# Performance work log

Measured on AMD Instinct MI355X. Metric: run time of the kernel, lower is better.

## Reference

```python
import jax, jax.numpy as jnp
import numpy as np

K = 16
NUM_CLASSES = 1000
TAU = 0.2
LOGIT_SCALE = 20.0


def setup_inputs() -> dict:
    key = jax.random.key(0)
    k1, k2, k3, k4, k5 = jax.random.split(key, 5)
    B, D, N = 2048, 256, 100000
    x = jax.random.normal(k1, (B, D), dtype=jnp.float32)
    mean = jax.random.normal(k2, (D,), dtype=jnp.float32)
    std = jax.random.uniform(k3, (D,), dtype=jnp.float32, minval=0.5, maxval=1.5)
    mem_features = jax.random.normal(k4, (N, D), dtype=jnp.float32)
    mem_labels = jax.random.randint(k5, (N,), 0, NUM_CLASSES)
    return {"x": x, "mean": mean, "std": std,
            "mem_features": mem_features, "mem_labels": mem_labels}


def reference(x, mean, std, mem_features, mem_labels):
    # preprocess: standardize then L2-normalize rows (eval mode, no noise)
    x = (x - mean) / std
    norm = jnp.maximum(jnp.linalg.norm(x, axis=1, keepdims=True), 1e-6)
    x = x / norm
    # dense cosine similarity: [B, N]
    sims = jnp.einsum('bd,nd->bn', x, mem_features)
    # top-k neighbors per query
    top_sims, top_idx = jax.lax.top_k(sims, K)          # [B, K]
    top_lbl = mem_labels[top_idx]                       # [B, K]
    weights = jax.nn.softmax(top_sims / max(1e-6, TAU), axis=1)
    # scatter-add softmax weights into class logits
    B = x.shape[0]
    rows = jnp.arange(B)[:, None]                       # [B, 1]
    logits = jnp.zeros((B, NUM_CLASSES), dtype=x.dtype).at[rows, top_lbl].add(weights)
    return logits * LOGIT_SCALE
```

## Files before the change

kernel.cpp:

```cpp
#include <hip/hip_runtime.h>
#include <math.h>

constexpr int BQ   = 2048;
constexpr int D    = 256;
constexpr int NMEM = 100000;
constexpr int TOPK = 16;
constexpr int NCLS = 1000;
constexpr float TAU = 0.2f;
constexpr float LOGIT_SCALE = 20.0f;

constexpr int KTOT = 256;
constexpr int BK   = 64;
constexpr int TM   = 128;
constexpr int TN   = 128;
constexpr int CTILES = 17;
constexpr int CHUNK  = TN * CTILES;
constexpr int NCH    = 48;
constexpr int RBLK   = BQ / TM;
constexpr int NBLK   = RBLK * NCH;
constexpr int TOTAL_IT = CTILES * (KTOT / BK);
constexpr float XSCALE = 16.0f;
constexpr float INV_XS = 0.0625f;
constexpr float THR    = 3.0f;
constexpr float THRS   = 48.0f;
constexpr int CAP    = 512;
constexpr int MSEL   = 64;
constexpr int SELCAP = 96;
constexpr float NEG  = -3.0e38f;

using i32x4  = __attribute__((ext_vector_type(4))) int;
using i32x8  = __attribute__((ext_vector_type(8))) int;
using f32x16 = __attribute__((ext_vector_type(16))) float;

__device__ __forceinline__ unsigned f2e4m3(float f) {
    const unsigned u = __float_as_uint(f);
    const unsigned s = (u >> 24) & 0x80u;
    const int e = (int)((u >> 23) & 0xff);
    int te = e - 120;
    if (te <= 0) return s;
    const unsigned m = u & 0x7fffffu;
    const unsigned r = m + 0x7ffffu + ((m >> 20) & 1u);
    unsigned keep;
    if (r & 0x800000u) { ++te; keep = 0; } else keep = (r >> 20) & 7u;
    if (te >= 16 || (te == 15 && keep == 7)) return s | 0x7eu;
    return s | ((unsigned)te << 3) | keep;
}

__device__ __forceinline__ void load_lds16(const void* g, void* l) {
    __builtin_amdgcn_global_load_lds((const __attribute__((address_space(1))) void*)g,
                                     (__attribute__((address_space(3))) void*)l,
                                     16, 0, 0);
}

__global__ __launch_bounds__(256) void knn_prep(
    const float* __restrict__ x, const float* __restrict__ mean,
    const float* __restrict__ stdv, unsigned char* __restrict__ A1,
    float* __restrict__ XN, int* __restrict__ cnt)
{
    const int row = blockIdx.x;
    const int t = threadIdx.x;
    float v = (x[row * D + t] - mean[t]) / stdv[t];
    float s = v * v;
    #pragma unroll
    for (int off = 32; off > 0; off >>= 1) s += __shfl_down(s, off, 64);
    __shared__ float wsum[4];
    __shared__ float nrm;
    const int lane = t & 63, wid = t >> 6;
    if (lane == 0) wsum[wid] = s;
    __syncthreads();
    if (t == 0) {
        nrm = fmaxf(sqrtf(wsum[0] + wsum[1] + wsum[2] + wsum[3]), 1e-6f);
        cnt[row] = 0;
    }
    __syncthreads();
    const float xnv = v / nrm;
    A1[(size_t)row * KTOT + t] = (unsigned char)f2e4m3(xnv * XSCALE);
    XN[(size_t)row * D + t] = xnv;
}

__global__ __launch_bounds__(256) void knn_convb(
    const float* __restrict__ mem, unsigned char* __restrict__ B1)
{
    const int tid = threadIdx.x;
    const int rloc = tid >> 5, t = tid & 31;
    const long n = (long)blockIdx.x * 8 + rloc;
    if (n >= NMEM) return;
    const float* src = mem + n * D + t * 8;
    const float4 v0 = *(const float4*)(src);
    const float4 v1 = *(const float4*)(src + 4);
    const float f[8] = {v0.x, v0.y, v0.z, v0.w, v1.x, v1.y, v1.z, v1.w};
    unsigned long long pk = 0;
    #pragma unroll
    for (int i = 0; i < 8; ++i)
        pk |= (unsigned long long)f2e4m3(f[i]) << (8 * i);
    *(unsigned long long*)(B1 + n * KTOT + t * 8) = pk;
}

__global__ __launch_bounds__(256, 3) void knn_gemm_topk(
    const unsigned char* __restrict__ A1, const unsigned char* __restrict__ B1,
    int* __restrict__ cnt, uint2* __restrict__ cand_buf)
{
    __shared__ alignas(16) unsigned char Bs[3][TN * BK];

    const int tid  = threadIdx.x;
    const int lane = tid & 63, wave = tid >> 6;
    const int wm = wave >> 1, wn = wave & 1;
    const int l31 = lane & 31;
    const int kb  = lane >> 5;

    const int nblk = blockIdx.x;
    const int xcd = nblk & 7, bi = nblk >> 3;
    const int rb = bi & 15;
    const int ch = (bi >> 4) + 6 * xcd;
    const int row0  = rb * TM;
    const int cbase = ch * CHUNK;

    i32x8 Areg[2][4];
    #pragma unroll
    for (int ti = 0; ti < 2; ++ti) {
        const unsigned char* ar =
            A1 + (size_t)(row0 + wm * 64 + ti * 32 + l31) * KTOT + kb * 32;
        #pragma unroll
        for (int ks = 0; ks < 4; ++ks) {
            const i32x4 lo = *(const i32x4*)(ar + ks * 64);
            const i32x4 hi = *(const i32x4*)(ar + ks * 64 + 16);
            Areg[ti][ks] = __builtin_shufflevector(lo, hi, 0, 1, 2, 3, 4, 5, 6, 7);
        }
    }

    int boff[2][2];
    #pragma unroll
    for (int tj = 0; tj < 2; ++tj) {
        const int br = wn * 64 + tj * 32 + l31;
        #pragma unroll
        for (int c = 0; c < 2; ++c)
            boff[tj][c] = br * BK + (((2 * kb + c) - (br >> 1)) & 3) * 16;
    }

    int cSub[2], bSeg[2];
    #pragma unroll
    for (int s = 0; s < 2; ++s) {
        const int ci = s * 256 + tid;
        const int r = ci >> 2, sl = ci & 3;
        cSub[s] = r;
        bSeg[s] = ((sl + (r >> 1)) & 3) << 4;
    }
    const unsigned char* bB[2];
    auto computeBB = [&](int tile) {
        #pragma unroll
        for (int s = 0; s < 2; ++s) {
            int candi = cbase + tile * TN + cSub[s];
            if (candi >= NMEM) candi = NMEM - 1;
            bB[s] = B1 + (size_t)candi * KTOT + bSeg[s];
        }
    };
    auto stageB = [&](int buf, int kofs) {
        #pragma unroll
        for (int s = 0; s < 2; ++s)
            load_lds16(bB[s] + kofs, (char*)Bs[buf] + s * 4096 + wave * 1024);
    };

    f32x16 acc[2][2];
    #pragma unroll
    for (int i = 0; i < 2; ++i)
        #pragma unroll
        for (int j = 0; j < 2; ++j)
            #pragma unroll
            for (int r = 0; r < 16; ++r) acc[i][j][r] = 0.f;

    computeBB(0);
    stageB(0, 0);
    stageB(1, 64);
    asm volatile("s_waitcnt vmcnt(2)" ::: "memory");
    __builtin_amdgcn_sched_barrier(0);
    __builtin_amdgcn_s_barrier();

    int p = 0;
    for (int t = 0; t < CTILES; ++t) {
        #pragma unroll
        for (int ks = 0; ks < 4; ++ks) {
            const int g = t * 4 + ks;

            const unsigned char* Bb = Bs[p];
            i32x8 Bfr[2];
            #pragma unroll
            for (int tj = 0; tj < 2; ++tj) {
                const i32x4 blo = *(const i32x4*)(Bb + boff[tj][0]);
                const i32x4 bhi = *(const i32x4*)(Bb + boff[tj][1]);
                Bfr[tj] = __builtin_shufflevector(blo, bhi, 0, 1, 2, 3, 4, 5, 6, 7);
            }

            const bool have2 = (g + 2 < TOTAL_IT);
            if (have2) {
                if (ks == 2) computeBB(t + 1);
                int pn = p + 2; if (pn >= 3) pn -= 3;
                stageB(pn, ((ks + 2) & 3) << 6);
            }

            #pragma unroll
            for (int ti = 0; ti < 2; ++ti)
                #pragma unroll
                for (int tj = 0; tj < 2; ++tj)
                    acc[ti][tj] = __builtin_amdgcn_mfma_scale_f32_32x32x64_f8f6f4(
                        Areg[ti][ks], Bfr[tj], acc[ti][tj], 0, 0,
                        0, 0x7f7f7f7f, 0, 0x7f7f7f7f);

            if (ks == 3) {
                const int tb = cbase + t * TN;
                #pragma unroll
                for (int ti = 0; ti < 2; ++ti) {
                    const int rb0 = row0 + wm * 64 + ti * 32 + 4 * kb;
                    #pragma unroll
                    for (int tj = 0; tj < 2; ++tj) {
                        const int cidx = tb + wn * 64 + tj * 32 + l31;
                        #pragma unroll
                        for (int r = 0; r < 16; ++r) {
                            const float v = acc[ti][tj][r];
                            if (v > THRS && cidx < NMEM) {
                                const int rg = rb0 + (r & 3) + 8 * (r >> 2);
                                const int pos = atomicAdd(&cnt[rg], 1);
                                if (pos < CAP)
                                    cand_buf[(size_t)rg * CAP + pos] =
                                        make_uint2(__float_as_uint(v * INV_XS),
                                                   (unsigned)cidx);
                            }
                            acc[ti][tj][r] = 0.f;
                        }
                    }
                }
            }

            if (g < TOTAL_IT - 1) {
                if (have2) {
                    asm volatile("s_waitcnt vmcnt(2)" ::: "memory");
                } else {
                    asm volatile("s_waitcnt vmcnt(0)" ::: "memory");
                }
                __builtin_amdgcn_sched_barrier(0);
                __builtin_amdgcn_s_barrier();
            }
            ++p; if (p >= 3) p = 0;
        }
    }
}

__global__ __launch_bounds__(256) void knn_final(
    const int* __restrict__ cnt, const uint2* __restrict__ cand_buf,
    const float* __restrict__ xn, const float* __restrict__ mem,
    const int* __restrict__ labels, float* __restrict__ out)
{
    constexpr float BSCALE = 200.0f;
    __shared__ float cls[NCLS];
    __shared__ uint2 cl[CAP];
    __shared__ int   hist[1024];
    __shared__ int   psum[256];
    __shared__ float tstar;
    __shared__ int   scount;
    __shared__ int   seli[SELCAP];
    __shared__ float ex[SELCAP];
    __shared__ float fs[TOPK];
    __shared__ int   fi[TOPK];
    __shared__ float zshare;

    const int row = blockIdx.x;
    const int tid = threadIdx.x;
    const int lane = tid & 63, w = tid >> 6;

    const float4 xr = *(const float4*)(xn + (size_t)row * D + lane * 4);

    for (int c = tid; c < NCLS; c += 256) cls[c] = 0.f;
    for (int i = tid; i < 1024; i += 256) hist[i] = 0;
    int n = cnt[row]; if (n > CAP) n = CAP;
    for (int i = tid; i < n; i += 256) cl[i] = cand_buf[(size_t)row * CAP + i];
    if (tid == 0) scount = 0;
    __syncthreads();

    for (int i = tid; i < n; i += 256) {
        const float v = __uint_as_float(cl[i].x);
        int b = (int)((v - THR) * BSCALE);
        b = max(0, min(1023, b));
        atomicAdd(&hist[b], 1);
    }
    __syncthreads();
    psum[tid] = hist[4 * tid] + hist[4 * tid + 1] + hist[4 * tid + 2] + hist[4 * tid + 3];
    __syncthreads();
    if (tid == 0) {
        int cum = 0, g = 255;
        for (; g >= 0; --g) {
            if (cum + psum[g] >= MSEL) break;
            cum += psum[g];
        }
        float t = THR;
        if (g >= 0) {
            int bb = 4 * g + 3;
            for (; bb > 4 * g; --bb) {
                cum += hist[bb];
                if (cum >= MSEL) break;
            }
            if (bb == 4 * g) cum += hist[bb];
            t = THR + (float)bb * (1.0f / BSCALE);
        }
        tstar = t;
    }
    __syncthreads();
    for (int i = tid; i < n; i += 256) {
        const float v = __uint_as_float(cl[i].x);
        if (v >= tstar) {
            const int p = atomicAdd(&scount, 1);
            if (p < SELCAP) seli[p] = (int)cl[i].y;
        }
    }
    __syncthreads();
    int ns = scount; if (ns > SELCAP) ns = SELCAP;

    for (int c = w; c < ns; c += 4) {
        const float4 mv = *(const float4*)(mem + (size_t)seli[c] * D + lane * 4);
        float s = xr.x * mv.x + xr.y * mv.y + xr.z * mv.z + xr.w * mv.w;
        #pragma unroll
        for (int off = 32; off > 0; off >>= 1) s += __shfl_down(s, off, 64);
        if (lane == 0) ex[c] = s;
    }
    __syncthreads();

    if (tid == 0) {
        float kmin = NEG; int kslot = 0;
        #pragma unroll
        for (int s = 0; s < TOPK; ++s) { fs[s] = NEG; fi[s] = -1; }
        for (int c = 0; c < ns; ++c) {
            const float v = ex[c];
            if (v > kmin) {
                fs[kslot] = v; fi[kslot] = seli[c];
                kmin = fs[0]; kslot = 0;
                #pragma unroll
                for (int s = 1; s < TOPK; ++s) {
                    const float tq = fs[s];
                    if (tq < kmin) { kmin = tq; kslot = s; }
                }
            }
        }
        float smax = fs[0];
        #pragma unroll
        for (int s = 1; s < TOPK; ++s) smax = fmaxf(smax, fs[s]);
        float e[TOPK]; float Z = 0.f;
        #pragma unroll
        for (int s = 0; s < TOPK; ++s) {
            e[s] = (fi[s] >= 0) ? expf((fs[s] - smax) * (1.0f / TAU)) : 0.f;
            Z += e[s];
        }
        for (int s = 0; s < TOPK; ++s) {
            if (fi[s] >= 0) cls[labels[fi[s]]] += e[s];
        }
        zshare = Z;
    }
    __syncthreads();
    const float scale = LOGIT_SCALE / zshare;
    for (int c = tid; c < NCLS; c += 256)
        out[(size_t)row * NCLS + c] = cls[c] * scale;
}

extern "C" void kernel_launch(void* const* d_in, const int* in_sizes, int n_in,
                              void* d_out, int out_size, void* d_ws, size_t ws_size,
                              hipStream_t stream) {
    (void)in_sizes; (void)n_in; (void)out_size; (void)ws_size;
    const float* x    = (const float*)d_in[0];
    const float* mean = (const float*)d_in[1];
    const float* stdv = (const float*)d_in[2];
    const float* mem  = (const float*)d_in[3];
    const int*   lbl  = (const int*)d_in[4];
    float* out = (float*)d_out;

    unsigned char* A1 = (unsigned char*)d_ws;
    float* XN = (float*)(A1 + (size_t)BQ * KTOT);
    unsigned char* B1 = (unsigned char*)(XN + (size_t)BQ * D);
    int* cnt = (int*)(B1 + (size_t)NMEM * KTOT);
    uint2* cand = (uint2*)(cnt + BQ);

    knn_prep<<<BQ, 256, 0, stream>>>(x, mean, stdv, A1, XN, cnt);
    knn_convb<<<(NMEM + 7) / 8, 256, 0, stream>>>(mem, B1);
    knn_gemm_topk<<<NBLK, 256, 0, stream>>>(A1, B1, cnt, cand);
    knn_final<<<BQ, 256, 0, stream>>>(cnt, cand, XN, mem, lbl, out);
}
```

Baseline: 420.7 us.

## Load B fragments directly from global into registers, drop LDS staging

The GEMM+threshold kernel stops staging memory-bank tiles through a triple-buffered LDS ring with barriers. Each wave now loads its B fragments straight from global into registers with a simple two-register double buffer. Blocks grow to 512 threads (8 waves, each owning 32 rows), and the chunk layout changes to 32 chunks of 25 tiles. This removes LDS traffic and block-wide barriers, at the cost of redundant global/L2 reads of B across waves and more exposed load latency without an explicit pipeline.

Result: slower. 466.9 us (+11.0%).

```diff
diff --git a/kernel.cpp b/kernel.cpp
--- a/kernel.cpp
+++ b/kernel.cpp
@@ -10,15 +10,13 @@
 constexpr float LOGIT_SCALE = 20.0f;
 
 constexpr int KTOT = 256;
-constexpr int BK   = 64;
 constexpr int TM   = 128;
 constexpr int TN   = 128;
-constexpr int CTILES = 17;
+constexpr int CTILES = 25;
 constexpr int CHUNK  = TN * CTILES;
-constexpr int NCH    = 48;
+constexpr int NCH    = 32;
 constexpr int RBLK   = BQ / TM;
 constexpr int NBLK   = RBLK * NCH;
-constexpr int TOTAL_IT = CTILES * (KTOT / BK);
 constexpr float XSCALE = 16.0f;
 constexpr float INV_XS = 0.0625f;
 constexpr float THR    = 3.0f;
@@ -44,12 +42,6 @@
     if (r & 0x800000u) { ++te; keep = 0; } else keep = (r >> 20) & 7u;
     if (te >= 16 || (te == 15 && keep == 7)) return s | 0x7eu;
     return s | ((unsigned)te << 3) | keep;
-}
-
-__device__ __forceinline__ void load_lds16(const void* g, void* l) {
-    __builtin_amdgcn_global_load_lds((const __attribute__((address_space(1))) void*)g,
-                                     (__attribute__((address_space(3))) void*)l,
-                                     16, 0, 0);
 }
 
 __global__ __launch_bounds__(256) void knn_prep(
@@ -96,12 +88,10 @@
     *(unsigned long long*)(B1 + n * KTOT + t * 8) = pk;
 }
 
-__global__ __launch_bounds__(256, 3) void knn_gemm_topk(
+__global__ __launch_bounds__(512, 4) void knn_gemm_topk(
     const unsigned char* __restrict__ A1, const unsigned char* __restrict__ B1,
     int* __restrict__ cnt, uint2* __restrict__ cand_buf)
 {
-    __shared__ alignas(16) unsigned char Bs[3][TN * BK];
-
     const int tid  = threadIdx.x;
     const int lane = tid & 63, wave = tid >> 6;
     const int wm = wave >> 1, wn = wave & 1;
@@ -111,135 +101,92 @@
     const int nblk = blockIdx.x;
     const int xcd = nblk & 7, bi = nblk >> 3;
     const int rb = bi & 15;
-    const int ch = (bi >> 4) + 6 * xcd;
+    const int ch = (bi >> 4) + 4 * xcd;
     const int row0  = rb * TM;
     const int cbase = ch * CHUNK;
 
-    i32x8 Areg[2][4];
-    #pragma unroll
-    for (int ti = 0; ti < 2; ++ti) {
+    i32x8 Areg[4];
+    {
         const unsigned char* ar =
-            A1 + (size_t)(row0 + wm * 64 + ti * 32 + l31) * KTOT + kb * 32;
+            A1 + (size_t)(row0 + wm * 32 + l31) * KTOT + kb * 32;
         #pragma unroll
         for (int ks = 0; ks < 4; ++ks) {
             const i32x4 lo = *(const i32x4*)(ar + ks * 64);
             const i32x4 hi = *(const i32x4*)(ar + ks * 64 + 16);
-            Areg[ti][ks] = __builtin_shufflevector(lo, hi, 0, 1, 2, 3, 4, 5, 6, 7);
-        }
-    }
-
-    int boff[2][2];
+            Areg[ks] = __builtin_shufflevector(lo, hi, 0, 1, 2, 3, 4, 5, 6, 7);
+        }
+    }
+
+    const int laneoff = wn * 64 + l31;
+    const unsigned char* bA[2];
+    auto computeBT = [&](int tile) {
+        const int tb = cbase + tile * TN;
+        #pragma unroll
+        for (int tj = 0; tj < 2; ++tj) {
+            int c = tb + laneoff + tj * 32;
+            if (c > NMEM - 1) c = NMEM - 1;
+            bA[tj] = B1 + ((size_t)c << 8) + kb * 32;
+        }
+    };
+    auto loadB = [&](int ksOfs, i32x8* dst) {
+        #pragma unroll
+        for (int tj = 0; tj < 2; ++tj) {
+            const i32x4 lo = *(const i32x4*)(bA[tj] + ksOfs);
+            const i32x4 hi = *(const i32x4*)(bA[tj] + ksOfs + 16);
+            dst[tj] = __builtin_shufflevector(lo, hi, 0, 1, 2, 3, 4, 5, 6, 7);
+        }
+    };
+
+    f32x16 acc[2];
     #pragma unroll
-    for (int tj = 0; tj < 2; ++tj) {
-        const int br = wn * 64 + tj * 32 + l31;
-        #pragma unroll
-        for (int c = 0; c < 2; ++c)
-            boff[tj][c] = br * BK + (((2 * kb + c) - (br >> 1)) & 3) * 16;
-    }
-
-    int cSub[2], bSeg[2];
-    #pragma unroll
-    for (int s = 0; s < 2; ++s) {
-        const int ci = s * 256 + tid;
-        const int r = ci >> 2, sl = ci & 3;
-        cSub[s] = r;
-        bSeg[s] = ((sl + (r >> 1)) & 3) << 4;
-    }
-    const unsigned char* bB[2];
-    auto computeBB = [&](int tile) {
-        #pragma unroll
-        for (int s = 0; s < 2; ++s) {
-            int candi = cbase + tile * TN + cSub[s];
-            if (candi >= NMEM) candi = NMEM - 1;
-            bB[s] = B1 + (size_t)candi * KTOT + bSeg[s];
-        }
-    };
-    auto stageB = [&](int buf, int kofs) {
-        #pragma unroll
-        for (int s = 0; s < 2; ++s)
-            load_lds16(bB[s] + kofs, (char*)Bs[buf] + s * 4096 + wave * 1024);
-    };
-
-    f32x16 acc[2][2];
-    #pragma unroll
-    for (int i = 0; i < 2; ++i)
-        #pragma unroll
-        for (int j = 0; j < 2; ++j)
+    for (int tj = 0; tj < 2; ++tj)
+        #pragma unroll
+        for (int r = 0; r < 16; ++r) acc[tj][r] = 0.f;
+
+    i32x8 Bb[2], Bc[2];
+    computeBT(0);
+    loadB(0, Bb);
+
+    for (int t = 0; t < CTILES; ++t) {
+        loadB(64, Bc);
+        #pragma unroll
+        for (int tj = 0; tj < 2; ++tj)
+            acc[tj] = __builtin_amdgcn_mfma_scale_f32_32x32x64_f8f6f4(
+                Areg[0], Bb[tj], acc[tj], 0, 0, 0, 0x7f7f7f7f, 0, 0x7f7f7f7f);
+        loadB(128, Bb);
+        #pragma unroll
+        for (int tj = 0; tj < 2; ++tj)
+            acc[tj] = __builtin_amdgcn_mfma_scale_f32_32x32x64_f8f6f4(
+                Areg[1], Bc[tj], acc[tj], 0, 0, 0, 0x7f7f7f7f, 0, 0x7f7f7f7f);
+        loadB(192, Bc);
+        #pragma unroll
+        for (int tj = 0; tj < 2; ++tj)
+            acc[tj] = __builtin_amdgcn_mfma_scale_f32_32x32x64_f8f6f4(
+                Areg[2], Bb[tj], acc[tj], 0, 0, 0, 0x7f7f7f7f, 0, 0x7f7f7f7f);
+        if (t + 1 < CTILES) { computeBT(t + 1); loadB(0, Bb); }
+        #pragma unroll
+        for (int tj = 0; tj < 2; ++tj)
+            acc[tj] = __builtin_amdgcn_mfma_scale_f32_32x32x64_f8f6f4(
+                Areg[3], Bc[tj], acc[tj], 0, 0, 0, 0x7f7f7f7f, 0, 0x7f7f7f7f);
+
+        const int tb = cbase + t * TN;
+        const int rb0 = row0 + wm * 32 + 4 * kb;
+        #pragma unroll
+        for (int tj = 0; tj < 2; ++tj) {
+            const int cidx = tb + wn * 64 + tj * 32 + l31;
             #pragma unroll
-            for (int r = 0; r < 16; ++r) acc[i][j][r] = 0.f;
-
-    computeBB(0);
-    stageB(0, 0);
-    stageB(1, 64);
-    asm volatile("s_waitcnt vmcnt(2)" ::: "memory");
-    __builtin_amdgcn_sched_barrier(0);
-    __builtin_amdgcn_s_barrier();
-
-    int p = 0;
-    for (int t = 0; t < CTILES; ++t) {
-        #pragma unroll
-        for (int ks = 0; ks < 4; ++ks) {
-            const int g = t * 4 + ks;
-
-            const unsigned char* Bb = Bs[p];
-            i32x8 Bfr[2];
-            #pragma unroll
-            for (int tj = 0; tj < 2; ++tj) {
-                const i32x4 blo = *(const i32x4*)(Bb + boff[tj][0]);
-                const i32x4 bhi = *(const i32x4*)(Bb + boff[tj][1]);
-                Bfr[tj] = __builtin_shufflevector(blo, bhi, 0, 1, 2, 3, 4, 5, 6, 7);
+            for (int r = 0; r < 16; ++r) {
+                const float v = acc[tj][r];
+                if (v > THRS && cidx < NMEM) {
+                    const int rg = rb0 + (r & 3) + 8 * (r >> 2);
+                    const int pos = atomicAdd(&cnt[rg], 1);
+                    if (pos < CAP)
+                        cand_buf[(size_t)rg * CAP + pos] =
+                            make_uint2(__float_as_uint(v * INV_XS),
+                                       (unsigned)cidx);
+                }
+                acc[tj][r] = 0.f;
             }
-
-            const bool have2 = (g + 2 < TOTAL_IT);
-            if (have2) {
-                if (ks == 2) computeBB(t + 1);
-                int pn = p + 2; if (pn >= 3) pn -= 3;
-                stageB(pn, ((ks + 2) & 3) << 6);
-            }
-
-            #pragma unroll
-            for (int ti = 0; ti < 2; ++ti)
-                #pragma unroll
-                for (int tj = 0; tj < 2; ++tj)
-                    acc[ti][tj] = __builtin_amdgcn_mfma_scale_f32_32x32x64_f8f6f4(
-                        Areg[ti][ks], Bfr[tj], acc[ti][tj], 0, 0,
-                        0, 0x7f7f7f7f, 0, 0x7f7f7f7f);
-
-            if (ks == 3) {
-                const int tb = cbase + t * TN;
-                #pragma unroll
-                for (int ti = 0; ti < 2; ++ti) {
-                    const int rb0 = row0 + wm * 64 + ti * 32 + 4 * kb;
-                    #pragma unroll
-                    for (int tj = 0; tj < 2; ++tj) {
-                        const int cidx = tb + wn * 64 + tj * 32 + l31;
-                        #pragma unroll
-                        for (int r = 0; r < 16; ++r) {
-                            const float v = acc[ti][tj][r];
-                            if (v > THRS && cidx < NMEM) {
-                                const int rg = rb0 + (r & 3) + 8 * (r >> 2);
-                                const int pos = atomicAdd(&cnt[rg], 1);
-                                if (pos < CAP)
-                                    cand_buf[(size_t)rg * CAP + pos] =
-                                        make_uint2(__float_as_uint(v * INV_XS),
-                                                   (unsigned)cidx);
-                            }
-                            acc[ti][tj][r] = 0.f;
-                        }
-                    }
-                }
-            }
-
-            if (g < TOTAL_IT - 1) {
-                if (have2) {
-                    asm volatile("s_waitcnt vmcnt(2)" ::: "memory");
-                } else {
-                    asm volatile("s_waitcnt vmcnt(0)" ::: "memory");
-                }
-                __builtin_amdgcn_sched_barrier(0);
-                __builtin_amdgcn_s_barrier();
-            }
-            ++p; if (p >= 3) p = 0;
         }
     }
 }
@@ -377,6 +324,6 @@
 
     knn_prep<<<BQ, 256, 0, stream>>>(x, mean, stdv, A1, XN, cnt);
     knn_convb<<<(NMEM + 7) / 8, 256, 0, stream>>>(mem, B1);
-    knn_gemm_topk<<<NBLK, 256, 0, stream>>>(A1, B1, cnt, cand);
+    knn_gemm_topk<<<NBLK, 512, 0, stream>>>(A1, B1, cnt, cand);
     knn_final<<<BQ, 256, 0, stream>>>(cnt, cand, XN, mem, lbl, out);
 }
```
